# Kernel tuning notes

Measured on AMD Instinct MI355X. Metric: run time of the kernel, lower is better.

## Reference

```python
import jax, jax.numpy as jnp
import numpy as np

B, S, D, H = 128, 512, 256, 256


def _lstm_cell(Wih, Whh, b, x_t, h, c):
    # PyTorch LSTM gate order: i, f, g, o. b = b_ih + b_hh (mathematically equivalent).
    z = x_t @ Wih.T + h @ Whh.T + b  # [B, 4H]
    i, f, g, o = jnp.split(z, 4, axis=-1)
    i = jax.nn.sigmoid(i)
    f = jax.nn.sigmoid(f)
    g = jnp.tanh(g)
    o = jax.nn.sigmoid(o)
    c = f * c + i * g
    h = o * jnp.tanh(c)
    return h, c


def setup_inputs() -> dict:
    key = jax.random.key(0)
    ks = jax.random.split(key, 12)
    s = 1.0 / np.sqrt(H)
    f32 = jnp.float32
    return {
        "x": jax.random.normal(ks[0], (B, S, D), f32),
        "enc_Wih": jax.random.uniform(ks[1], (4 * H, D), f32, -s, s),
        "enc_Whh": jax.random.uniform(ks[2], (4 * H, H), f32, -s, s),
        "enc_b": jax.random.uniform(ks[3], (4 * H,), f32, -s, s),
        "dec_Wih": jax.random.uniform(ks[4], (4 * H, D), f32, -s, s),
        "dec_Whh": jax.random.uniform(ks[5], (4 * H, H), f32, -s, s),
        "dec_b": jax.random.uniform(ks[6], (4 * H,), f32, -s, s),
        "W1_w": jax.random.uniform(ks[7], (H, H), f32, -s, s),
        "W1_b": jax.random.uniform(ks[8], (H,), f32, -s, s),
        "W2_w": jax.random.uniform(ks[9], (H, H), f32, -s, s),
        "W2_b": jax.random.uniform(ks[10], (H,), f32, -s, s),
        "vt_w": jax.random.uniform(ks[11], (H,), f32, -s, s),
    }


def reference(x, enc_Wih, enc_Whh, enc_b, dec_Wih, dec_Whh, dec_b,
              W1_w, W1_b, W2_w, W2_b, vt_w):
    b_, s_, d_ = x.shape
    h0 = jnp.zeros((b_, H), x.dtype)
    c0 = jnp.zeros((b_, H), x.dtype)

    # ---- encoder LSTM over time ----
    def enc_step(carry, x_t):
        h, c = carry
        h, c = _lstm_cell(enc_Wih, enc_Whh, enc_b, x_t, h, c)
        return (h, c), h

    (h, c), enc_out = jax.lax.scan(enc_step, (h0, c0), jnp.swapaxes(x, 0, 1))
    enc_out = jnp.swapaxes(enc_out, 0, 1)  # [B, S, H]

    # W1(encoder_outputs) is loop-invariant; compute once (same math as original)
    enc_proj = enc_out @ W1_w.T + W1_b  # [B, S, H]

    # ---- pointer decode loop ----
    def dec_step(carry, _):
        h, c, din = carry
        h, c = _lstm_cell(dec_Wih, dec_Whh, dec_b, din, h, c)
        q = h @ W2_w.T + W2_b  # [B, H]
        u = jnp.einsum('bsh,h->bs', jnp.tanh(enc_proj + q[:, None, :]), vt_w)
        probs = jax.nn.softmax(u, axis=1)  # [B, S]
        din = jnp.einsum('bs,bsh->bh', probs, enc_out)
        return (h, c, din), probs

    din0 = jnp.zeros((b_, d_), x.dtype)
    _, probs_seq = jax.lax.scan(dec_step, (h, c, din0), None, length=s_)
    return jnp.swapaxes(probs_seq, 0, 1)  # [B, S, S]
```

## Files before the change

kernel.cpp:

```cpp
#include <hip/hip_runtime.h>
#include <hip/hip_fp16.h>

typedef _Float16 h2_t __attribute__((ext_vector_type(2)));
typedef unsigned int u32x4 __attribute__((ext_vector_type(4)));

#define KEXP 2.8853900817779268f

#define BARRIER() do { \
    asm volatile("s_waitcnt lgkmcnt(0)" ::: "memory"); \
    __builtin_amdgcn_s_barrier(); \
    asm volatile("" ::: "memory"); \
} while (0)

__device__ __forceinline__ float fdot2(unsigned int a, unsigned int b, float c) {
#if __has_builtin(__builtin_amdgcn_fdot2)
    return __builtin_amdgcn_fdot2(__builtin_bit_cast(h2_t, a), __builtin_bit_cast(h2_t, b), c, false);
#else
    h2_t ha = __builtin_bit_cast(h2_t, a), hb = __builtin_bit_cast(h2_t, b);
    return c + (float)ha[0]*(float)hb[0] + (float)ha[1]*(float)hb[1];
#endif
}

__device__ __forceinline__ float dot4(u32x4 a, u32x4 b, float c) {
    c = fdot2(a[0], b[0], c); c = fdot2(a[1], b[1], c);
    c = fdot2(a[2], b[2], c); c = fdot2(a[3], b[3], c);
    return c;
}

__device__ __forceinline__ unsigned int pk16(float a, float b) {
    auto h = __builtin_amdgcn_cvt_pkrtz(a, b);
    return __builtin_bit_cast(unsigned int, h);
}

__device__ __forceinline__ float rcp_(float x) {
#if __has_builtin(__builtin_amdgcn_rcpf)
    return __builtin_amdgcn_rcpf(x);
#else
    return 1.0f / x;
#endif
}

__device__ __forceinline__ float sigm(float x) { return rcp_(1.0f + __expf(-x)); }
__device__ __forceinline__ float tanh_(float x) {
    float e = __expf(2.0f * x);
    return 1.0f - 2.0f * rcp_(e + 1.0f);
}

__device__ __forceinline__ unsigned int rcp1p2exp(unsigned int s) {
    __half2 e = h2exp2(__builtin_bit_cast(__half2, s));
    __half2 d = __hadd2(e, __float2half2_rn(1.0f));
    return __builtin_bit_cast(unsigned int, h2rcp(d));
}
__device__ __forceinline__ unsigned int hadd2u(unsigned int a, unsigned int b) {
    return __builtin_bit_cast(unsigned int,
        __hadd2(__builtin_bit_cast(__half2, a), __builtin_bit_cast(__half2, b)));
}

__device__ __forceinline__ void st_u32(unsigned int* p, unsigned int v) {
    __hip_atomic_store(p, v, __ATOMIC_RELAXED, __HIP_MEMORY_SCOPE_AGENT);
}
__device__ __forceinline__ unsigned int ld_u32(const unsigned int* p) {
    return __hip_atomic_load(p, __ATOMIC_RELAXED, __HIP_MEMORY_SCOPE_AGENT);
}
__device__ __forceinline__ float ld_f32(const unsigned int* p) {
    return __builtin_bit_cast(float, ld_u32(p));
}
__device__ __forceinline__ float h2f_lo(unsigned int v) {
    return __half2float(__ushort_as_half((unsigned short)(v & 0xffffu)));
}
__device__ __forceinline__ float h2f_hi(unsigned int v) {
    return __half2float(__ushort_as_half((unsigned short)(v >> 16)));
}

__global__ void init_flags_kernel(unsigned int* flags) {
    flags[threadIdx.x * 32] = 0u;
}

__global__ __launch_bounds__(256) void prep_kernel(
    const float* __restrict__ encWhh, const float* __restrict__ decWih,
    const float* __restrict__ decWhh, const float* __restrict__ W2w,
    u32x4* __restrict__ We8, u32x4* __restrict__ Wi8, u32x4* __restrict__ Wh8, u32x4* __restrict__ W28)
{
    int id = blockIdx.x * 256 + threadIdx.x;
    if (id < 3 * 32768) {
        int mat = id >> 15, local = id & 32767;
        int j = local & 1023, k8 = local >> 10;
        const float* src = mat == 0 ? encWhh : (mat == 1 ? decWih : decWhh);
        u32x4* dst = mat == 0 ? We8 : (mat == 1 ? Wi8 : Wh8);
        const float* p = src + (size_t)j * 256 + k8 * 8;
        float4 a = *(const float4*)p; float4 c = *(const float4*)(p + 4);
        u32x4 v; v[0] = pk16(a.x, a.y); v[1] = pk16(a.z, a.w);
        v[2] = pk16(c.x, c.y); v[3] = pk16(c.z, c.w);
        dst[k8 * 1024 + j] = v;
    } else {
        int local = id - 3 * 32768;
        if (local < 8192) {
            int m = local & 255, k8 = local >> 8;
            const float* p = W2w + (size_t)m * 256 + k8 * 8;
            float4 a = *(const float4*)p; float4 c = *(const float4*)(p + 4);
            u32x4 v; v[0] = pk16(a.x, a.y); v[1] = pk16(a.z, a.w);
            v[2] = pk16(c.x, c.y); v[3] = pk16(c.z, c.w);
            W28[k8 * 256 + m] = v;
        }
    }
}

template<int A_IS_F16, int TR_OUT>
__global__ __launch_bounds__(256) void gemm_kernel(
    const void* __restrict__ A_, const float* __restrict__ Bw,
    const float* __restrict__ bias, unsigned short* __restrict__ C, int N, float scale)
{
    __shared__ float As[16][68];
    __shared__ float Bs[16][132];
    const int t = threadIdx.x;
    const int row0 = blockIdx.y * 64, col0 = blockIdx.x * 128;
    const int ty = t >> 4, tx = t & 15;
    const int lm = t & 63, lkq = t >> 6;
    const int ln = t & 127, lkq2 = t >> 7;
    float acc[4][8] = {};
    for (int k0 = 0; k0 < 256; k0 += 16) {
        float4 av;
        if constexpr (A_IS_F16) {
            const unsigned short* A = (const unsigned short*)A_;
            uint2 ha = *(const uint2*)(A + (size_t)(row0 + lm) * 256 + k0 + lkq * 4);
            h2_t h0 = __builtin_bit_cast(h2_t, ha.x);
            h2_t h1 = __builtin_bit_cast(h2_t, ha.y);
            av = make_float4((float)h0[0], (float)h0[1], (float)h1[0], (float)h1[1]);
        } else {
            av = *(const float4*)((const float*)A_ + (size_t)(row0 + lm) * 256 + k0 + lkq * 4);
        }
        const float* bp = Bw + (size_t)(col0 + ln) * 256 + k0 + lkq2 * 8;
        float4 bv0 = *(const float4*)bp;
        float4 bv1 = *(const float4*)(bp + 4);
        __syncthreads();
        As[lkq * 4 + 0][lm] = av.x;
        As[lkq * 4 + 1][lm] = av.y;
        As[lkq * 4 + 2][lm] = av.z;
        As[lkq * 4 + 3][lm] = av.w;
        Bs[lkq2 * 8 + 0][ln] = bv0.x;
        Bs[lkq2 * 8 + 1][ln] = bv0.y;
        Bs[lkq2 * 8 + 2][ln] = bv0.z;
        Bs[lkq2 * 8 + 3][ln] = bv0.w;
        Bs[lkq2 * 8 + 4][ln] = bv1.x;
        Bs[lkq2 * 8 + 5][ln] = bv1.y;
        Bs[lkq2 * 8 + 6][ln] = bv1.z;
        Bs[lkq2 * 8 + 7][ln] = bv1.w;
        __syncthreads();
        #pragma unroll
        for (int kk = 0; kk < 16; ++kk) {
            float4 a = *(float4*)&As[kk][ty * 4];
            float4 b0 = *(float4*)&Bs[kk][tx * 8];
            float4 b1 = *(float4*)&Bs[kk][tx * 8 + 4];
            float ar[4] = {a.x, a.y, a.z, a.w};
            float br[8] = {b0.x, b0.y, b0.z, b0.w, b1.x, b1.y, b1.z, b1.w};
            #pragma unroll
            for (int i = 0; i < 4; ++i)
                #pragma unroll
                for (int j = 0; j < 8; ++j)
                    acc[i][j] = fmaf(ar[i], br[j], acc[i][j]);
        }
    }
    float bv[8];
    #pragma unroll
    for (int j = 0; j < 8; ++j) bv[j] = bias[col0 + tx * 8 + j];
    #pragma unroll
    for (int i = 0; i < 4; ++i) {
        unsigned int w0 = pk16((acc[i][0] + bv[0]) * scale, (acc[i][1] + bv[1]) * scale);
        unsigned int w1 = pk16((acc[i][2] + bv[2]) * scale, (acc[i][3] + bv[3]) * scale);
        unsigned int w2 = pk16((acc[i][4] + bv[4]) * scale, (acc[i][5] + bv[5]) * scale);
        unsigned int w3 = pk16((acc[i][6] + bv[6]) * scale, (acc[i][7] + bv[7]) * scale);
        uint4 val = make_uint4(w0, w1, w2, w3);
        if constexpr (TR_OUT) {
            int rr = row0 + ty * 4 + i;
            int bb = rr >> 9, s = rr & 511;
            int c8 = (col0 >> 3) + tx;
            ((uint4*)C)[(size_t)bb * 16384 + (size_t)c8 * 512 + s] = val;
        } else {
            *(uint4*)(C + (size_t)(row0 + ty * 4 + i) * N + col0 + tx * 8) = val;
        }
    }
}

__global__ __launch_bounds__(1024) void encoder_kernel(
    const unsigned short* __restrict__ Xproj, const u32x4* __restrict__ We8,
    float* __restrict__ hfin, float* __restrict__ cfin,
    unsigned short* __restrict__ enc_h, unsigned int* __restrict__ encT,
    unsigned int* __restrict__ xg, unsigned int* __restrict__ eflags)
{
    const int blk = blockIdx.x;
    const int b = blk & 127, r = blk >> 7;
    const int t = threadIdx.x;
    __shared__ __align__(16) float zs[1024];
    __shared__ __align__(16) unsigned int hh2[128];
    if (t < 128) hh2[t] = 0u;
    float c_reg = 0.f, hprev = 0.f, hcur = 0.f;
    __syncthreads();

    const int jl = t & 511, kh = t >> 9;
    const u32x4* wp = We8 + (size_t)(kh * 16) * 1024 + r * 512 + jl;
    const unsigned short* xp = Xproj + (size_t)b * 524288 + r * 512 + jl;
    const int fo_me = (b * 2 + r) * 32, fo_pr = (b * 2 + (1 - r)) * 32;
    unsigned int* xg_me = xg + (b * 2 + r) * 512;
    const unsigned int* xg_pr = xg + (b * 2 + (1 - r)) * 512;

    for (int step = 0; step < 512; ++step) {
        float acc = (kh == 0)
            ? __half2float(__ushort_as_half(__builtin_nontemporal_load(xp + (size_t)step * 1024)))
            : 0.f;
        #pragma unroll 8
        for (int i = 0; i < 16; ++i) {
            u32x4 wv = wp[i * 1024];
            u32x4 hv = *(const u32x4*)&hh2[(kh * 16 + i) * 4];
            acc = dot4(wv, hv, acc);
        }
        zs[t] = acc;
        BARRIER();
        float ga = 0.f, gb = 0.f;
        if (t < 256) {
            float z_a = zs[t] + zs[t + 512];
            float z_b = zs[t + 256] + zs[t + 768];
            if (r == 0) { ga = sigm(z_a); gb = sigm(z_b); }
            else        { ga = tanh_(z_a); gb = sigm(z_b); }
            st_u32(&xg_me[t], __builtin_bit_cast(unsigned int, ga));
            st_u32(&xg_me[256 + t], __builtin_bit_cast(unsigned int, gb));
            asm volatile("s_waitcnt vmcnt(0)" ::: "memory");
        }
        BARRIER();
        if (t == 0) {
            unsigned int T = (unsigned)(step + 1);
            st_u32(&eflags[fo_me], T);
            while (ld_u32(&eflags[fo_pr]) < T) __builtin_amdgcn_s_sleep(1);
        }
        BARRIER();
        if (t < 256) {
            float oa = ld_f32(&xg_pr[t]);
            float ob = ld_f32(&xg_pr[256 + t]);
            float gi, gf, gg, go_;
            if (r == 0) { gi = ga; gf = gb; gg = oa; go_ = ob; }
            else        { gg = ga; go_ = gb; gi = oa; gf = ob; }
            c_reg = gf * c_reg + gi * gg;
            float h = go_ * tanh_(c_reg);
            float hnb = __shfl_down(h, 1);
            if (!(t & 1)) hh2[t >> 1] = pk16(h, hnb);
            if (r == 0) {
                __builtin_nontemporal_store(__half_as_ushort(__float2half_rn(h)),
                                            enc_h + (size_t)(b * 512 + step) * 256 + t);
            } else {
                if (step & 1) {
                    int s2 = step >> 1;
                    encT[(size_t)b * 65536 + (size_t)((s2 >> 2) * 256 + t) * 4 + (s2 & 3)] = pk16(hprev, h);
                }
                hprev = h;
            }
            hcur = h;
        }
        BARRIER();
    }
    if (r == 0 && t < 256) { hfin[b * 256 + t] = hcur; cfin[b * 256 + t] = c_reg; }
}

__global__ __launch_bounds__(1024) void decoder_kernel(
    const u32x4* __restrict__ Wi8, const u32x4* __restrict__ Wh8, const u32x4* __restrict__ W28,
    const float* __restrict__ dec_b, const float* __restrict__ W2b, const float* __restrict__ vtw,
    const float* __restrict__ hfin, const float* __restrict__ cfin,
    const u32x4* __restrict__ projT, const u32x4* __restrict__ encT,
    unsigned int* __restrict__ xgate, unsigned int* __restrict__ xdin,
    unsigned int* __restrict__ xsum, unsigned int* __restrict__ flags,
    float* __restrict__ out)
{
    const int blk = blockIdx.x;
    const int b = blk & 127, r = blk >> 7;
    const int t = threadIdx.x;
    const int lane = t & 63, w = t >> 6;

    __shared__ __align__(16) float zs[1024];
    __shared__ __align__(16) unsigned int hh2[128];
    __shared__ __align__(16) unsigned int din2[128];
    __shared__ __align__(16) unsigned int qp2[128];
    __shared__ __align__(16) unsigned int mv2u[128];
    __shared__ __align__(16) unsigned int p2u[128];
    __shared__ float wreds[16];
    __shared__ float svtS, rsS;

    const int fo_me = (b * 2 + r) * 32, fo_pr = (b * 2 + (1 - r)) * 32;
    const int go_me = (b * 2 + r) * 256, go_pr = (b * 2 + (1 - r)) * 256;

    float c_reg = (t < 256) ? cfin[b * 256 + t] : 0.f;
    const float bja = (t < 256) ? dec_b[r * 512 + t] : 0.f;
    const float bjb = (t < 256) ? dec_b[r * 512 + 256 + t] : 0.f;
    const float w2b_r = (t < 256) ? W2b[t] : 0.f;
    if (t < 128) { din2[t] = 0u; mv2u[t] = pk16(-2.f * vtw[2 * t], -2.f * vtw[2 * t + 1]); }
    if (t < 256) zs[t] = vtw[t];
    __syncthreads();
    if (t < 64) {
        float v = zs[t] + zs[t + 64] + zs[t + 128] + zs[t + 192];
        #pragma unroll
        for (int off = 1; off < 64; off <<= 1) v += __shfl_xor(v, off);
        if (t == 0) svtS = v;
    }
    if (t < 256) {
        float h0 = hfin[b * 256 + t];
        float hnb = __shfl_down(h0, 1);
        if (!(t & 1)) hh2[t >> 1] = pk16(h0, hnb);
    }
    __syncthreads();
    const float svt = svtS;

    const int jl = t & 511, kh = t >> 9;
    const u32x4* wp = (kh ? Wh8 : Wi8) + (r * 512 + jl);
    const unsigned int* vls = kh ? (const unsigned int*)hh2 : (const unsigned int*)din2;
    const int hF = t & 255, slF = t >> 8;
    const int sl4 = t >> 2, qr = t & 3;
    const int s_g = r * 256 + sl4;
    const u32x4* pD = projT + (size_t)b * 16384 + (size_t)(qr * 8) * 512 + s_g;
    const u32x4* fD = encT + (size_t)b * 16384 + (size_t)(r * 32 + slF * 8) * 256 + hF;
    float* outp = out + (size_t)b * 262144;

    for (int step = 0; step < 512; ++step) {
        float acc = 0.f;
        #pragma unroll 8
        for (int k8 = 0; k8 < 32; ++k8) {
            u32x4 wv = wp[k8 * 1024];
            u32x4 hv = *(const u32x4*)&vls[k8 * 4];
            acc = dot4(wv, hv, acc);
        }
        zs[t] = acc;
        BARRIER();
        unsigned int myg = 0u;
        if (t < 256) {
            float z_a = bja + zs[t] + zs[t + 512];
            float z_b = bjb + zs[t + 256] + zs[t + 768];
            float ga, gb;
            if (r == 0) { ga = sigm(z_a); gb = sigm(z_b); }
            else        { ga = tanh_(z_a); gb = sigm(z_b); }
            myg = (unsigned int)__half_as_ushort(__float2half_rn(ga)) |
                  ((unsigned int)__half_as_ushort(__float2half_rn(gb)) << 16);
            st_u32(&xgate[go_me + t], myg);
            asm volatile("s_waitcnt vmcnt(0)" ::: "memory");
        }
        BARRIER();
        if (t == 0) {
            unsigned int T = (unsigned)(2 * step + 1);
            st_u32(&flags[fo_me], T);
            while (ld_u32(&flags[fo_pr]) < T) __builtin_amdgcn_s_sleep(1);
        }
        BARRIER();
        if (t < 256) {
            unsigned int og = ld_u32(&xgate[go_pr + t]);
            float la = h2f_lo(myg), lb = h2f_hi(myg);
            float oa = h2f_lo(og),  ob = h2f_hi(og);
            float gi, gf, gg, go_;
            if (r == 0) { gi = la; gf = lb; gg = oa; go_ = ob; }
            else        { gg = la; go_ = lb; gi = oa; gf = ob; }
            c_reg = gf * c_reg + gi * gg;
            float h = go_ * tanh_(c_reg);
            float hnb = __shfl_down(h, 1);
            if (!(t & 1)) hh2[t >> 1] = pk16(h, hnb);
        }
        BARRIER();
        {
            float qa = 0.f;
            #pragma unroll
            for (int i = 0; i < 8; ++i) {
                int k8 = slF * 8 + i;
                u32x4 wv = W28[k8 * 256 + hF];
                u32x4 hv = *(const u32x4*)&hh2[k8 * 4];
                qa = dot4(wv, hv, qa);
            }
            zs[t] = qa;
        }
        BARRIER();
        if (t < 256) {
            float q = (w2b_r + zs[t] + zs[t + 256] + zs[t + 512] + zs[t + 768]) * KEXP;
            float qnx = __shfl_down(q, 1);
            if (!(t & 1)) qp2[t >> 1] = pk16(q, qnx);
        }
        BARRIER();
        float e;
        u32x4 fv[8];
        {
            float up = 0.f;
            #pragma unroll 4
            for (int i = 0; i < 8; ++i) {
                u32x4 pv = pD[i * 512];
                int c = qr * 8 + i;
                u32x4 qh = *(const u32x4*)&qp2[c * 4];
                u32x4 mv = *(const u32x4*)&mv2u[c * 4];
                up = fdot2(mv[0], rcp1p2exp(hadd2u(pv[0], qh[0])), up);
                up = fdot2(mv[1], rcp1p2exp(hadd2u(pv[1], qh[1])), up);
                up = fdot2(mv[2], rcp1p2exp(hadd2u(pv[2], qh[2])), up);
                up = fdot2(mv[3], rcp1p2exp(hadd2u(pv[3], qh[3])), up);
            }
            up += __shfl_xor(up, 1);
            up += __shfl_xor(up, 2);
            e = __expf(up + svt);
            #pragma unroll
            for (int j = 0; j < 8; ++j) fv[j] = fD[j * 256];
            float enx = __shfl_down(e, 4);
            if (!(t & 7)) p2u[t >> 3] = pk16(e, enx);
            float ws = e;
            #pragma unroll
            for (int off = 1; off < 64; off <<= 1) ws += __shfl_xor(ws, off);
            if (lane == 0) wreds[w] = ws;
        }
        BARRIER();
        {
            float fa = 0.f;
            #pragma unroll
            for (int j = 0; j < 8; ++j) {
                u32x4 ev = fv[j];
                u32x4 pw = *(const u32x4*)&p2u[(slF * 8 + j) * 4];
                fa = dot4(ev, pw, fa);
            }
            zs[t] = fa;
        }
        BARRIER();
        float dpart = 0.f;
        if (t < 256) {
            dpart = zs[t] + zs[t + 256] + zs[t + 512] + zs[t + 768];
            st_u32(&xdin[go_me + t], __builtin_bit_cast(unsigned int, dpart));
            asm volatile("s_waitcnt vmcnt(0)" ::: "memory");
        }
        BARRIER();
        if (t == 0) {
            float ls = 0.f;
            #pragma unroll
            for (int k = 0; k < 16; ++k) ls += wreds[k];
            ls *= 0.25f;
            st_u32(&xsum[fo_me], __builtin_bit_cast(unsigned int, ls));
            asm volatile("s_waitcnt vmcnt(0)" ::: "memory");
            unsigned int T = (unsigned)(2 * step + 2);
            st_u32(&flags[fo_me], T);
            while (ld_u32(&flags[fo_pr]) < T) __builtin_amdgcn_s_sleep(1);
            float lr = __builtin_bit_cast(float, ld_u32(&xsum[fo_pr]));
            rsS = rcp_(ls + lr);
        }
        BARRIER();
        {
            float rs = rsS;
            if (t < 256) {
                float drem = __builtin_bit_cast(float, ld_u32(&xdin[go_pr + t]));
                float dval = (dpart + drem) * rs;
                float dnx = __shfl_down(dval, 1);
                if (!(t & 1)) din2[t >> 1] = pk16(dval, dnx);
            }
            if ((t & 3) == 0) outp[(size_t)step * 512 + s_g] = e * rs;
        }
        BARRIER();
    }
}

extern "C" void kernel_launch(void* const* d_in, const int* in_sizes, int n_in,
                              void* d_out, int out_size, void* d_ws, size_t ws_size,
                              hipStream_t stream) {
    const float* x      = (const float*)d_in[0];
    const float* encWih = (const float*)d_in[1];
    const float* encWhh = (const float*)d_in[2];
    const float* enc_b  = (const float*)d_in[3];
    const float* decWih = (const float*)d_in[4];
    const float* decWhh = (const float*)d_in[5];
    const float* dec_bp = (const float*)d_in[6];
    const float* W1w    = (const float*)d_in[7];
    const float* W1b    = (const float*)d_in[8];
    const float* W2w    = (const float*)d_in[9];
    const float* W2bp   = (const float*)d_in[10];
    const float* vtw    = (const float*)d_in[11];

    char* ws = (char*)d_ws;
    u32x4* We8 = (u32x4*)(ws);
    u32x4* Wi8 = (u32x4*)(ws + 524288);
    u32x4* Wh8 = (u32x4*)(ws + 1048576);
    u32x4* W28 = (u32x4*)(ws + 1572864);
    unsigned short* enc_h = (unsigned short*)(ws + 1703936);
    unsigned int*   encT  = (unsigned int*)(ws + 35258368);
    unsigned short* projT = (unsigned short*)(ws + 68812800);
    float* hfin = (float*)(ws + 102367232);
    float* cfin = (float*)(ws + 102498304);

    unsigned int* flags = (unsigned int*)(ws + 1703936);
    unsigned int* xsum  = (unsigned int*)(ws + 1703936 + 32768);
    unsigned int* xgate = (unsigned int*)(ws + 1703936 + 65536);
    unsigned int* xdin  = (unsigned int*)(ws + 1703936 + 65536 + 262144);

    unsigned int* eflags = (unsigned int*)(ws + 68812800);
    unsigned int* exg    = (unsigned int*)(ws + 68812800 + 32768);

    unsigned short* Xproj = (unsigned short*)d_out;

    prep_kernel<<<416, 256, 0, stream>>>(encWhh, decWih, decWhh, W2w, We8, Wi8, Wh8, W28);
    gemm_kernel<0, 0><<<dim3(8, 1024), 256, 0, stream>>>(x, encWih, enc_b, Xproj, 1024, 1.0f);
    init_flags_kernel<<<1, 256, 0, stream>>>(eflags);
    encoder_kernel<<<256, 1024, 0, stream>>>(Xproj, We8, hfin, cfin, enc_h, (unsigned int*)encT,
                                             exg, eflags);
    gemm_kernel<1, 1><<<dim3(2, 1024), 256, 0, stream>>>(enc_h, W1w, W1b, projT, 256, KEXP);
    init_flags_kernel<<<1, 256, 0, stream>>>(flags);
    decoder_kernel<<<256, 1024, 0, stream>>>(Wi8, Wh8, W28, dec_bp, W2bp, vtw,
                                             hfin, cfin, (const u32x4*)projT, (const u32x4*)encT,
                                             xgate, xdin, xsum, flags, (float*)d_out);
}
```

Before: 13.73 ms.

## Split LSTM hidden units across block pair instead of gate halves

Each block of the two-block pair now computes all four gates for its own 128 hidden units rather than half the gates for all 256 units. It can then finish the cell update locally and exchange only packed fp16 hidden values (64 words) with its partner instead of gate activations. This shrinks the cross-block exchange payload and shortens the serial work after the flag wait, at the cost of an extra barrier to merge the partner's hidden half into shared memory. Both the encoder and decoder recurrences are restructured, and the decoder's input and hidden weight loops are separated so the bias can seed the accumulator.

```diff
diff --git a/kernel.cpp b/kernel.cpp
--- a/kernel.cpp
+++ b/kernel.cpp
@@ -185,7 +185,7 @@
     const unsigned short* __restrict__ Xproj, const u32x4* __restrict__ We8,
     float* __restrict__ hfin, float* __restrict__ cfin,
     unsigned short* __restrict__ enc_h, unsigned int* __restrict__ encT,
-    unsigned int* __restrict__ xg, unsigned int* __restrict__ eflags)
+    unsigned int* __restrict__ xh, unsigned int* __restrict__ eflags)
 {
     const int blk = blockIdx.x;
     const int b = blk & 127, r = blk >> 7;
@@ -193,15 +193,17 @@
     __shared__ __align__(16) float zs[1024];
     __shared__ __align__(16) unsigned int hh2[128];
     if (t < 128) hh2[t] = 0u;
-    float c_reg = 0.f, hprev = 0.f, hcur = 0.f;
+    float c_reg = 0.f;
+    unsigned int hprev_u = 0u;
     __syncthreads();
 
     const int jl = t & 511, kh = t >> 9;
-    const u32x4* wp = We8 + (size_t)(kh * 16) * 1024 + r * 512 + jl;
-    const unsigned short* xp = Xproj + (size_t)b * 524288 + r * 512 + jl;
+    const int rowA = ((jl >> 7) << 8) + r * 128 + (jl & 127);
+    const u32x4* wp = We8 + (size_t)(kh * 16) * 1024 + rowA;
+    const unsigned short* xp = Xproj + (size_t)b * 524288 + rowA;
     const int fo_me = (b * 2 + r) * 32, fo_pr = (b * 2 + (1 - r)) * 32;
-    unsigned int* xg_me = xg + (b * 2 + r) * 512;
-    const unsigned int* xg_pr = xg + (b * 2 + (1 - r)) * 512;
+    unsigned int* xh_me = xh + (b * 2 + r) * 512;
+    const unsigned int* xh_pr = xh + (b * 2 + (1 - r)) * 512;
 
     for (int step = 0; step < 512; ++step) {
         float acc = (kh == 0)
@@ -215,14 +217,19 @@
         }
         zs[t] = acc;
         BARRIER();
-        float ga = 0.f, gb = 0.f;
-        if (t < 256) {
-            float z_a = zs[t] + zs[t + 512];
-            float z_b = zs[t + 256] + zs[t + 768];
-            if (r == 0) { ga = sigm(z_a); gb = sigm(z_b); }
-            else        { ga = tanh_(z_a); gb = sigm(z_b); }
-            st_u32(&xg_me[t], __builtin_bit_cast(unsigned int, ga));
-            st_u32(&xg_me[256 + t], __builtin_bit_cast(unsigned int, gb));
+        if (t < 128) {
+            float gi = sigm(zs[t] + zs[t + 512]);
+            float gf = sigm(zs[128 + t] + zs[640 + t]);
+            float gg = tanh_(zs[256 + t] + zs[768 + t]);
+            float go_ = sigm(zs[384 + t] + zs[896 + t]);
+            c_reg = gf * c_reg + gi * gg;
+            float h = go_ * tanh_(c_reg);
+            float hnb = __shfl_down(h, 1);
+            if (!(t & 1)) {
+                unsigned int hp = pk16(h, hnb);
+                hh2[r * 64 + (t >> 1)] = hp;
+                st_u32(&xh_me[t >> 1], hp);
+            }
             asm volatile("s_waitcnt vmcnt(0)" ::: "memory");
         }
         BARRIER();
@@ -232,31 +239,31 @@
             while (ld_u32(&eflags[fo_pr]) < T) __builtin_amdgcn_s_sleep(1);
         }
         BARRIER();
+        if (t < 64) hh2[(1 - r) * 64 + t] = ld_u32(&xh_pr[t]);
+        BARRIER();
         if (t < 256) {
-            float oa = ld_f32(&xg_pr[t]);
-            float ob = ld_f32(&xg_pr[256 + t]);
-            float gi, gf, gg, go_;
-            if (r == 0) { gi = ga; gf = gb; gg = oa; go_ = ob; }
-            else        { gg = ga; go_ = gb; gi = oa; gf = ob; }
-            c_reg = gf * c_reg + gi * gg;
-            float h = go_ * tanh_(c_reg);
-            float hnb = __shfl_down(h, 1);
-            if (!(t & 1)) hh2[t >> 1] = pk16(h, hnb);
+            unsigned int hp = hh2[t >> 1];
+            unsigned int hv16 = (t & 1) ? (hp >> 16) : (hp & 0xffffu);
             if (r == 0) {
-                __builtin_nontemporal_store(__half_as_ushort(__float2half_rn(h)),
+                __builtin_nontemporal_store((unsigned short)hv16,
                                             enc_h + (size_t)(b * 512 + step) * 256 + t);
             } else {
                 if (step & 1) {
                     int s2 = step >> 1;
-                    encT[(size_t)b * 65536 + (size_t)((s2 >> 2) * 256 + t) * 4 + (s2 & 3)] = pk16(hprev, h);
+                    encT[(size_t)b * 65536 + (size_t)((s2 >> 2) * 256 + t) * 4 + (s2 & 3)] =
+                        hprev_u | (hv16 << 16);
                 }
-                hprev = h;
-            }
-            hcur = h;
-        }
-        BARRIER();
-    }
-    if (r == 0 && t < 256) { hfin[b * 256 + t] = hcur; cfin[b * 256 + t] = c_reg; }
+                hprev_u = hv16;
+            }
+        }
+        BARRIER();
+    }
+    if (t < 128) {
+        unsigned int hp = hh2[r * 64 + (t >> 1)];
+        float hv = (t & 1) ? h2f_hi(hp) : h2f_lo(hp);
+        hfin[b * 256 + r * 128 + t] = hv;
+        cfin[b * 256 + r * 128 + t] = c_reg;
+    }
 }
 
 __global__ __launch_bounds__(1024) void decoder_kernel(
@@ -285,9 +292,7 @@
     const int fo_me = (b * 2 + r) * 32, fo_pr = (b * 2 + (1 - r)) * 32;
     const int go_me = (b * 2 + r) * 256, go_pr = (b * 2 + (1 - r)) * 256;
 
-    float c_reg = (t < 256) ? cfin[b * 256 + t] : 0.f;
-    const float bja = (t < 256) ? dec_b[r * 512 + t] : 0.f;
-    const float bjb = (t < 256) ? dec_b[r * 512 + 256 + t] : 0.f;
+    float c_reg = (t < 128) ? cfin[b * 256 + r * 128 + t] : 0.f;
     const float w2b_r = (t < 256) ? W2b[t] : 0.f;
     if (t < 128) { din2[t] = 0u; mv2u[t] = pk16(-2.f * vtw[2 * t], -2.f * vtw[2 * t + 1]); }
     if (t < 256) zs[t] = vtw[t];
@@ -307,8 +312,10 @@
     const float svt = svtS;
 
     const int jl = t & 511, kh = t >> 9;
-    const u32x4* wp = (kh ? Wh8 : Wi8) + (r * 512 + jl);
-    const unsigned int* vls = kh ? (const unsigned int*)hh2 : (const unsigned int*)din2;
+    const int rowA = ((jl >> 7) << 8) + r * 128 + (jl & 127);
+    const float bseed = (kh == 0) ? dec_b[rowA] : 0.f;
+    const u32x4* wpi = Wi8 + rowA;
+    const u32x4* wph = Wh8 + rowA;
     const int hF = t & 255, slF = t >> 8;
     const int sl4 = t >> 2, qr = t & 3;
     const int s_g = r * 256 + sl4;
@@ -317,25 +324,34 @@
     float* outp = out + (size_t)b * 262144;
 
     for (int step = 0; step < 512; ++step) {
-        float acc = 0.f;
+        float acc = bseed;
         #pragma unroll 8
-        for (int k8 = 0; k8 < 32; ++k8) {
-            u32x4 wv = wp[k8 * 1024];
-            u32x4 hv = *(const u32x4*)&vls[k8 * 4];
+        for (int k8 = 0; k8 < 16; ++k8) {
+            u32x4 wv = wpi[(kh * 16 + k8) * 1024];
+            u32x4 dv = *(const u32x4*)&din2[(kh * 16 + k8) * 4];
+            acc = dot4(wv, dv, acc);
+        }
+        #pragma unroll 8
+        for (int k8 = 0; k8 < 16; ++k8) {
+            u32x4 wv = wph[(kh * 16 + k8) * 1024];
+            u32x4 hv = *(const u32x4*)&hh2[(kh * 16 + k8) * 4];
             acc = dot4(wv, hv, acc);
         }
         zs[t] = acc;
         BARRIER();
-        unsigned int myg = 0u;
-        if (t < 256) {
-            float z_a = bja + zs[t] + zs[t + 512];
-            float z_b = bjb + zs[t + 256] + zs[t + 768];
-            float ga, gb;
-            if (r == 0) { ga = sigm(z_a); gb = sigm(z_b); }
-            else        { ga = tanh_(z_a); gb = sigm(z_b); }
-            myg = (unsigned int)__half_as_ushort(__float2half_rn(ga)) |
-                  ((unsigned int)__half_as_ushort(__float2half_rn(gb)) << 16);
-            st_u32(&xgate[go_me + t], myg);
+        if (t < 128) {
+            float gi = sigm(zs[t] + zs[t + 512]);
+            float gf = sigm(zs[128 + t] + zs[640 + t]);
+            float gg = tanh_(zs[256 + t] + zs[768 + t]);
+            float go_ = sigm(zs[384 + t] + zs[896 + t]);
+            c_reg = gf * c_reg + gi * gg;
+            float h = go_ * tanh_(c_reg);
+            float hnb = __shfl_down(h, 1);
+            if (!(t & 1)) {
+                unsigned int hp = pk16(h, hnb);
+                hh2[r * 64 + (t >> 1)] = hp;
+                st_u32(&xgate[go_me + (t >> 1)], hp);
+            }
             asm volatile("s_waitcnt vmcnt(0)" ::: "memory");
         }
         BARRIER();
@@ -345,18 +361,7 @@
             while (ld_u32(&flags[fo_pr]) < T) __builtin_amdgcn_s_sleep(1);
         }
         BARRIER();
-        if (t < 256) {
-            unsigned int og = ld_u32(&xgate[go_pr + t]);
-            float la = h2f_lo(myg), lb = h2f_hi(myg);
-            float oa = h2f_lo(og),  ob = h2f_hi(og);
-            float gi, gf, gg, go_;
-            if (r == 0) { gi = la; gf = lb; gg = oa; go_ = ob; }
-            else        { gg = la; go_ = lb; gi = oa; gf = ob; }
-            c_reg = gf * c_reg + gi * gg;
-            float h = go_ * tanh_(c_reg);
-            float hnb = __shfl_down(h, 1);
-            if (!(t & 1)) hh2[t >> 1] = pk16(h, hnb);
-        }
+        if (t < 64) hh2[(1 - r) * 64 + t] = ld_u32(&xgate[go_pr + t]);
         BARRIER();
         {
             float qa = 0.f;
@@ -483,7 +488,7 @@
     unsigned int* xdin  = (unsigned int*)(ws + 1703936 + 65536 + 262144);
 
     unsigned int* eflags = (unsigned int*)(ws + 68812800);
-    unsigned int* exg    = (unsigned int*)(ws + 68812800 + 32768);
+    unsigned int* exh    = (unsigned int*)(ws + 68812800 + 32768);
 
     unsigned short* Xproj = (unsigned short*)d_out;
 
@@ -491,7 +496,7 @@
     gemm_kernel<0, 0><<<dim3(8, 1024), 256, 0, stream>>>(x, encWih, enc_b, Xproj, 1024, 1.0f);
     init_flags_kernel<<<1, 256, 0, stream>>>(eflags);
     encoder_kernel<<<256, 1024, 0, stream>>>(Xproj, We8, hfin, cfin, enc_h, (unsigned int*)encT,
-                                             exg, eflags);
+                                             exh, eflags);
     gemm_kernel<1, 1><<<dim3(2, 1024), 256, 0, stream>>>(enc_h, W1w, W1b, projT, 256, KEXP);
     init_flags_kernel<<<1, 256, 0, stream>>>(flags);
     decoder_kernel<<<256, 1024, 0, stream>>>(Wi8, Wh8, W28, dec_bp, W2bp, vtw,
```

Result: no change. 13.64 ms, median of 2 (-0.7%).
